# Performance work log

Measured on AMD Instinct MI355X. Metric: run time of the kernel, lower is better.

## Reference

```python
import jax, jax.numpy as jnp
import numpy as np

KH = KW = 5   # kernel_size
STRIDE = 1
PAD = 2


def _unfold(x, kh, kw, stride, pad):
    """Replicates F.unfold: returns (B, C*kh*kw, L) with channel slowest,
    then (i, j) within the kernel window (same ordering as torch)."""
    B, C, H, W = x.shape
    xp = jnp.pad(x, ((0, 0), (0, 0), (pad, pad), (pad, pad)))
    Ho = (H + 2 * pad - kh) // stride + 1
    Wo = (W + 2 * pad - kw) // stride + 1
    cols = []
    for i in range(kh):          # small fixed loop over kernel offsets (25 iters)
        for j in range(kw):
            cols.append(xp[:, :, i:i + stride * Ho:stride, j:j + stride * Wo:stride])
    # (B, C, kh*kw, Ho, Wo) -> (B, C*kh*kw, L)
    patches = jnp.stack(cols, axis=2)
    return patches.reshape(B, C * kh * kw, Ho * Wo), Ho, Wo


def setup_inputs() -> dict:
    key = jax.random.key(0)
    k1, k2 = jax.random.split(key)
    x = jax.random.normal(k1, (32, 3, 224, 224), dtype=jnp.float32)
    # kaiming_uniform-style init for weight (out_channels, in_ch*kh*kw)
    fan_in = 3 * KH * KW
    bound = np.sqrt(6.0 / fan_in)  # kaiming_uniform with a=sqrt(5) default gain approx
    weight = jax.random.uniform(k2, (64, fan_in), dtype=jnp.float32,
                                minval=-bound, maxval=bound)
    return {"x": x, "weight": weight}


def reference(x, weight):
    """RBF_Conv2d._cdist: euclidean distance between each receptive-field
    window and each prototype row of `weight`.
    x: (B, C, H, W), weight: (O, D=C*kh*kw) -> out: (B, O, Ho, Wo)."""
    B = x.shape[0]
    O = weight.shape[0]
    windows, Ho, Wo = _unfold(x, KH, KW, STRIDE, PAD)   # (B, D, L)
    windows = windows.transpose(0, 2, 1)                # (B, L, D)
    # cdist via ||p||^2 + ||w||^2 - 2 p.w (same trick torch.cdist uses)
    pn = jnp.sum(windows * windows, axis=-1)            # (B, L)
    wn = jnp.sum(weight * weight, axis=-1)              # (O,)
    dots = jnp.einsum('bld,od->blo', windows, weight)   # (B, L, O)
    d2 = pn[:, :, None] + wn[None, None, :] - 2.0 * dots
    dist = jnp.sqrt(jnp.maximum(d2, 0.0))               # (B, L, O)
    return dist.transpose(0, 2, 1).reshape(B, O, Ho, Wo)
```

## Files before the change

kernel.cpp:

```cpp
#include <hip/hip_runtime.h>
#include <hip/hip_bf16.h>
#include <math.h>


#define KH 5
#define KW 5
#define PAD 2
#define CH 3
#define DD 75
#define OC 64
#define HH 224
#define WW 224
#define HW (HH * WW)
#define NSX 7

using short8_t = __attribute__((ext_vector_type(8))) short;
using f32x16   = __attribute__((ext_vector_type(16))) float;

union Oct { unsigned int w[4]; short8_t v; };

__device__ inline unsigned int rne_bf16(float v) {
    return (unsigned int)__builtin_bit_cast(unsigned short, __float2bfloat16(v));
}

__device__ inline float fsqrt_fast(float x) {
    float r;
    asm("v_sqrt_f32 %0, %1" : "=v"(r) : "v"(x));
    return r;
}

template<bool EDGE>
__device__ inline float xelem(const float* __restrict__ xb, int y, int xp, int d) {
    if (d >= DD) return 0.f;
    const int c = d / 25, rem = d % 25, i = rem / 5, j = rem % 5;
    int gy = y + i - PAD;
    int gx = xp + j;
    if constexpr (!EDGE) {
        return xb[(c * HH + gy) * WW + gx];
    } else {
        bool ok = ((unsigned)gy < (unsigned)HH) & ((unsigned)gx < (unsigned)WW);
        int gyc = min(max(gy, 0), HH - 1);
        int gxc = min(max(gx, 0), WW - 1);
        float raw = xb[(c * HH + gyc) * WW + gxc];
        return ok ? raw : 0.f;
    }
}

template<int D0, bool EDGE>
__device__ inline void build_oct_rne(const float* __restrict__ xb, int y, int xp,
                                     float& pn, Oct& b) {
#pragma unroll
    for (int rr = 0; rr < 8; rr += 2) {
        float v0 = xelem<EDGE>(xb, y, xp, D0 + rr);
        float v1 = xelem<EDGE>(xb, y, xp, D0 + rr + 1);
        pn = fmaf(v0, v0, pn);
        pn = fmaf(v1, v1, pn);
        b.w[rr >> 1] = rne_bf16(v0) | (rne_bf16(v1) << 16);
    }
}

template<int D0>
__device__ inline void build_aoct_wn(const float* wrow, Oct& a, float& wns) {
#pragma unroll
    for (int rr = 0; rr < 8; rr += 2) {
        float r0 = (D0 + rr     < DD) ? wrow[D0 + rr]     : 0.f;
        float r1 = (D0 + rr + 1 < DD) ? wrow[D0 + rr + 1] : 0.f;
        wns = fmaf(r0, r0, wns);
        wns = fmaf(r1, r1, wns);
        a.w[rr >> 1] = rne_bf16(-2.f * r0) | (rne_bf16(-2.f * r1) << 16);
    }
}

#define MFMA(A, B, C) __builtin_amdgcn_mfma_f32_32x32x16_bf16((A), (B), (C), 0, 0, 0)

template<bool EDGE>
__device__ inline void do_strip(const float* __restrict__ xb, int y, int xp, int hi,
                                const Oct (&ah)[2][5], float* __restrict__ op) {
    float pnp = 0.f;
    Oct bh[5];
    if (hi == 0) {
        build_oct_rne<0,  EDGE>(xb, y, xp, pnp, bh[0]);
        build_oct_rne<16, EDGE>(xb, y, xp, pnp, bh[1]);
        build_oct_rne<32, EDGE>(xb, y, xp, pnp, bh[2]);
        build_oct_rne<48, EDGE>(xb, y, xp, pnp, bh[3]);
        build_oct_rne<64, EDGE>(xb, y, xp, pnp, bh[4]);
    } else {
        build_oct_rne<8,  EDGE>(xb, y, xp, pnp, bh[0]);
        build_oct_rne<24, EDGE>(xb, y, xp, pnp, bh[1]);
        build_oct_rne<40, EDGE>(xb, y, xp, pnp, bh[2]);
        build_oct_rne<56, EDGE>(xb, y, xp, pnp, bh[3]);
        build_oct_rne<72, EDGE>(xb, y, xp, pnp, bh[4]);
    }
    float pn = pnp + __shfl_xor(pnp, 32);
    if (hi == 1) {
        unsigned int up  = __builtin_bit_cast(unsigned int, pn);
        float pnhv = __builtin_bit_cast(float, up & 0xFFFF0000u);
        unsigned int pnl = rne_bf16(pn - pnhv);
        bh[4].w[1] |= 0x3F800000u;
        bh[4].w[2]  = 0x3F80u | (up & 0xFFFF0000u);
        bh[4].w[3]  = pnl;
    }

    f32x16 acc0 = {0.f,0.f,0.f,0.f,0.f,0.f,0.f,0.f,0.f,0.f,0.f,0.f,0.f,0.f,0.f,0.f};
    f32x16 acc1 = acc0;
#pragma unroll
    for (int st = 0; st < 5; ++st) {
        acc0 = MFMA(ah[0][st].v, bh[st].v, acc0);
        acc1 = MFMA(ah[1][st].v, bh[st].v, acc1);
    }

#pragma unroll
    for (int reg = 0; reg < 16; ++reg) {
        int ob = (reg & 3) + 8 * (reg >> 2);
        op[(size_t)ob * HW]        = fsqrt_fast(fmaxf(acc0[reg], 0.f));
        op[(size_t)(ob + 32) * HW] = fsqrt_fast(fmaxf(acc1[reg], 0.f));
    }
}

__global__ __launch_bounds__(256, 4) void rbf_mfma(const float* __restrict__ x,
                                                   const float* __restrict__ w,
                                                   float* __restrict__ out,
                                                   int nstrips, int nwaves) {
    __shared__ float wlds[OC * DD];
    const int tid  = threadIdx.x;

    for (int idx = tid; idx < OC * DD; idx += 256)
        wlds[idx] = w[idx];
    __syncthreads();

    const int lane = tid & 63;
    const int l31  = lane & 31;
    const int hi   = lane >> 5;

    float wnp[2] = {0.f, 0.f};
    Oct ah[2][5];
    if (hi == 0) {
#pragma unroll
        for (int mt = 0; mt < 2; ++mt) {
            const float* wrow = wlds + (l31 + 32 * mt) * DD;
            build_aoct_wn<0 >(wrow, ah[mt][0], wnp[mt]);
            build_aoct_wn<16>(wrow, ah[mt][1], wnp[mt]);
            build_aoct_wn<32>(wrow, ah[mt][2], wnp[mt]);
            build_aoct_wn<48>(wrow, ah[mt][3], wnp[mt]);
            build_aoct_wn<64>(wrow, ah[mt][4], wnp[mt]);
        }
    } else {
#pragma unroll
        for (int mt = 0; mt < 2; ++mt) {
            const float* wrow = wlds + (l31 + 32 * mt) * DD;
            build_aoct_wn<8 >(wrow, ah[mt][0], wnp[mt]);
            build_aoct_wn<24>(wrow, ah[mt][1], wnp[mt]);
            build_aoct_wn<40>(wrow, ah[mt][2], wnp[mt]);
            build_aoct_wn<56>(wrow, ah[mt][3], wnp[mt]);
            build_aoct_wn<72>(wrow, ah[mt][4], wnp[mt]);
        }
    }
    float wn0 = wnp[0] + __shfl_xor(wnp[0], 32);
    float wn1 = wnp[1] + __shfl_xor(wnp[1], 32);
    if (hi == 1) {
#pragma unroll
        for (int mt = 0; mt < 2; ++mt) {
            float wnv = mt ? wn1 : wn0;
            unsigned int uwn = __builtin_bit_cast(unsigned int, wnv);
            float wnhv = __builtin_bit_cast(float, uwn & 0xFFFF0000u);
            unsigned int wnl = rne_bf16(wnv - wnhv);
            ah[mt][4].w[1] = (ah[mt][4].w[1] & 0xFFFFu) | (uwn & 0xFFFF0000u);
            ah[mt][4].w[2] = wnl | (0x3F80u << 16);
            ah[mt][4].w[3] = 0x3F80u;
        }
    }

    const int gw = blockIdx.x * 4 + (tid >> 6);
    for (int s = gw; s < nstrips; s += nwaves) {
        int sx = s % NSX;
        int t  = s / NSX;
        int y  = t % HH;
        int b  = t / HH;
        int x0 = sx * 32;
        const float* xb = x + (size_t)b * (CH * HW);
        int xp = x0 + l31 - PAD;
        float* op = out + (size_t)b * OC * HW + (size_t)(y * WW + x0 + l31)
                        + (size_t)hi * 4 * HW;
        bool interior = (y >= PAD) & (y < HH - PAD) & (sx >= 1) & (sx <= 5);
        if (interior) do_strip<false>(xb, y, xp, hi, ah, op);
        else          do_strip<true >(xb, y, xp, hi, ah, op);
    }
}

extern "C" void kernel_launch(void* const* d_in, const int* in_sizes, int n_in,
                              void* d_out, int out_size, void* d_ws, size_t ws_size,
                              hipStream_t stream) {
    const float* x = (const float*)d_in[0];
    const float* w = (const float*)d_in[1];
    float* out     = (float*)d_out;

    int B       = in_sizes[0] / (CH * HW);
    int nstrips = B * HH * NSX;
    int nblocks = 1024;
    int nwaves  = nblocks * 4;

    rbf_mfma<<<nblocks, 256, 0, stream>>>(x, w, out, nstrips, nwaves);
}
```

Measured before the change: 139.2 us.

## Assign each block a contiguous band of seven rows per image

Replaces the grid-stride strip loop with a fixed mapping: each block handles 7 consecutive output rows of one batch image (49 strips split across 4 waves), launching B*32 blocks. This keeps a block's input reads within a small row band, improving cache reuse of overlapping 5x5 windows, and removes the div/mod index math. It hardcodes B-dependent grid sizing and an uneven wave split, and now depends on HH being a multiple of 7*32.

Result: faster. 113.4 us (median of 2 runs) (-18.5%).

```diff
diff --git a/kernel.cpp b/kernel.cpp
--- a/kernel.cpp
+++ b/kernel.cpp
@@ -13,6 +13,7 @@
 #define WW 224
 #define HW (HH * WW)
 #define NSX 7
+#define RPB 7
 
 using short8_t = __attribute__((ext_vector_type(8))) short;
 using f32x16   = __attribute__((ext_vector_type(16))) float;
@@ -119,8 +120,7 @@
 
 __global__ __launch_bounds__(256, 4) void rbf_mfma(const float* __restrict__ x,
                                                    const float* __restrict__ w,
-                                                   float* __restrict__ out,
-                                                   int nstrips, int nwaves) {
+                                                   float* __restrict__ out) {
     __shared__ float wlds[OC * DD];
     const int tid  = threadIdx.x;
 
@@ -170,17 +170,22 @@
         }
     }
 
-    const int gw = blockIdx.x * 4 + (tid >> 6);
-    for (int s = gw; s < nstrips; s += nwaves) {
-        int sx = s % NSX;
-        int t  = s / NSX;
-        int y  = t % HH;
-        int b  = t / HH;
-        int x0 = sx * 32;
-        const float* xb = x + (size_t)b * (CH * HW);
-        int xp = x0 + l31 - PAD;
-        float* op = out + (size_t)b * OC * HW + (size_t)(y * WW + x0 + l31)
-                        + (size_t)hi * 4 * HW;
+    const int b  = blockIdx.x >> 5;
+    const int y0 = (blockIdx.x & 31) * RPB;
+    const int wv = tid >> 6;
+    const float* xb = x + (size_t)b * (CH * HW);
+    float* outb = out + (size_t)b * OC * HW + (size_t)hi * 4 * HW + l31;
+
+    const int niter = (wv == 0) ? 13 : 12;
+#pragma unroll 1
+    for (int it = 0; it < niter; ++it) {
+        int sidx = it * 4 + wv;
+        int r    = (sidx * 37) >> 8;
+        int sx   = sidx - r * 7;
+        int y    = y0 + r;
+        int x0   = sx * 32;
+        int xp   = x0 + l31 - PAD;
+        float* op = outb + (size_t)y * WW + x0;
         bool interior = (y >= PAD) & (y < HH - PAD) & (sx >= 1) & (sx <= 5);
         if (interior) do_strip<false>(xb, y, xp, hi, ah, op);
         else          do_strip<true >(xb, y, xp, hi, ah, op);
@@ -195,9 +200,7 @@
     float* out     = (float*)d_out;
 
     int B       = in_sizes[0] / (CH * HW);
-    int nstrips = B * HH * NSX;
-    int nblocks = 1024;
-    int nwaves  = nblocks * 4;
-
-    rbf_mfma<<<nblocks, 256, 0, stream>>>(x, w, out, nstrips, nwaves);
-}
+    int nblocks = B * 32;
+
+    rbf_mfma<<<nblocks, 256, 0, stream>>>(x, w, out);
+}
```
